# Performance work log

Measured on AMD Instinct MI355X. Metric: run time of the kernel, lower is better.

Reference implementation:

```python
import jax, jax.numpy as jnp
import numpy as np

D_MODEL = 256
EXPERT_DIM = 512
NUM_EXPERTS = 8
TOP_K = 2
SEQ_LEN = 2048
BATCH = 2


def setup_inputs() -> dict:
    key = jax.random.key(0)
    ks = jax.random.split(key, 8)
    s = 0.02
    x = jax.random.normal(ks[0], (SEQ_LEN, BATCH, D_MODEL), dtype=jnp.float32)
    # gate: torch Linear(d_model, num_experts); store as [d, E] so logits = x @ Wg + bg
    Wg = jax.random.normal(ks[1], (D_MODEL, NUM_EXPERTS), dtype=jnp.float32) * s
    bg = jax.random.normal(ks[2], (NUM_EXPERTS,), dtype=jnp.float32) * s
    bias = jnp.zeros((NUM_EXPERTS,), dtype=jnp.float32)  # dynamic routing bias
    # experts: Linear(d, h) -> ReLU -> Linear(h, d), stacked over E
    W1 = jax.random.normal(ks[3], (NUM_EXPERTS, D_MODEL, EXPERT_DIM), dtype=jnp.float32) * s
    b1 = jax.random.normal(ks[4], (NUM_EXPERTS, EXPERT_DIM), dtype=jnp.float32) * s
    W2 = jax.random.normal(ks[5], (NUM_EXPERTS, EXPERT_DIM, D_MODEL), dtype=jnp.float32) * s
    b2 = jax.random.normal(ks[6], (NUM_EXPERTS, D_MODEL), dtype=jnp.float32) * s
    return {"x": x, "Wg": Wg, "bg": bg, "bias": bias, "W1": W1, "b1": b1, "W2": W2, "b2": b2}


def reference(x, Wg, bg, bias, W1, b1, W2, b2):
    # x: [seq, batch, d] -> flatten tokens
    x_flat = x.reshape(-1, D_MODEL)                      # [T, d]
    gate_logits = x_flat @ Wg + bg + bias                # [T, E]
    topk_vals, topk_idx = jax.lax.top_k(gate_logits, TOP_K)   # [T, K]
    # torch code subtracts the row max (topk_vals[:, :1], sorted desc) then softmaxes;
    # jax.nn.softmax is the same stable computation.
    topk_w = jax.nn.softmax(topk_vals, axis=-1)          # [T, K]
    # combine weights over experts: zero for unchosen experts -> exact same math
    # as the masked gather + scatter-add in the original loop.
    combine = (jax.nn.one_hot(topk_idx, NUM_EXPERTS, dtype=x.dtype)
               * topk_w[..., None]).sum(axis=1)          # [T, E]
    h = jax.nn.relu(jnp.einsum('td,edh->teh', x_flat, W1) + b1)   # [T, E, H]
    y = jnp.einsum('teh,ehd->ted', h, W2) + b2                     # [T, E, d]
    out = jnp.einsum('ted,te->td', y, combine)                     # [T, d]
    # dropout is identity in eval mode (p applied only in training)
    return out.reshape(x.shape)
```

## Files before the change

kernel.cpp:

```cpp
#include <hip/hip_runtime.h>
#include <hip/hip_bf16.h>
#include <math.h>

#define D_MODEL 256
#define EXPERT_DIM 512
#define NUM_EXPERTS 8
#define T_TOKENS 4096
#define TM 64
#define NGB 32
#define XS_LD 264

typedef unsigned short ushort_t;
typedef short short8_t __attribute__((ext_vector_type(8)));
typedef float f32x4 __attribute__((ext_vector_type(4)));

__device__ __forceinline__ ushort_t f2bf(float f) {
    unsigned int u = __float_as_uint(f);
    u += 0x7FFFu + ((u >> 16) & 1u);
    return (ushort_t)(u >> 16);
}

__global__ __launch_bounds__(256) void prep_kernel(
    const float* __restrict__ x, const float* __restrict__ Wg,
    const float* __restrict__ bg, const float* __restrict__ bias,
    const float* __restrict__ W1, const float* __restrict__ W2,
    ushort_t* __restrict__ W1f, ushort_t* __restrict__ W2f,
    ushort_t* __restrict__ xb,
    int* __restrict__ gcounts, int* __restrict__ lists,
    float* __restrict__ wts, int* __restrict__ slots)
{
    __shared__ float xs[128][33];
    __shared__ float accbuf[128][9];
    __shared__ int lcount[NUM_EXPERTS];

    const int tid = threadIdx.x;
    if (blockIdx.x < NGB) {
        const int gb = blockIdx.x;
        const int tbase = gb * 128;
        const int tl = tid & 127;
        const int kh = tid >> 7;
        if (tid < NUM_EXPERTS) lcount[tid] = 0;
        float acc[NUM_EXPERTS];
#pragma unroll
        for (int e = 0; e < NUM_EXPERTS; ++e) acc[e] = 0.f;

        for (int kc = 0; kc < 8; ++kc) {
            __syncthreads();
#pragma unroll
            for (int it = 0; it < 4; ++it) {
                int pos = it * 256 + tid;
                int r = pos >> 3, c4 = pos & 7;
                const float* src = x + (size_t)(tbase + r) * D_MODEL + kc * 32 + c4 * 4;
                float4 v = *(const float4*)src;
                xs[r][c4 * 4 + 0] = v.x; xs[r][c4 * 4 + 1] = v.y;
                xs[r][c4 * 4 + 2] = v.z; xs[r][c4 * 4 + 3] = v.w;
                ushort4 o;
                o.x = f2bf(v.x); o.y = f2bf(v.y); o.z = f2bf(v.z); o.w = f2bf(v.w);
                *(ushort4*)&xb[(size_t)(tbase + r) * D_MODEL + kc * 32 + c4 * 4] = o;
            }
            __syncthreads();
            for (int k = kh * 16; k < kh * 16 + 16; ++k) {
                float xv = xs[tl][k];
                const float* wr = Wg + (kc * 32 + k) * NUM_EXPERTS;
#pragma unroll
                for (int e = 0; e < NUM_EXPERTS; ++e) acc[e] += xv * wr[e];
            }
        }
        __syncthreads();
        if (kh == 1) {
#pragma unroll
            for (int e = 0; e < NUM_EXPERTS; ++e) accbuf[tl][e] = acc[e];
        }
        __syncthreads();
        if (kh == 0) {
            float v0 = -3.0e38f, v1 = -3.0e38f; int i0 = 0, i1 = 0;
#pragma unroll
            for (int e = 0; e < NUM_EXPERTS; ++e) {
                float v = acc[e] + accbuf[tl][e] + bg[e] + bias[e];
                if (v > v0) { v1 = v0; i1 = i0; v0 = v; i0 = e; }
                else if (v > v1) { v1 = v; i1 = e; }
            }
            float e1 = __expf(v1 - v0);
            float inv = 1.f / (1.f + e1);
            float w0 = inv, w1 = e1 * inv;

            int p0 = atomicAdd(&lcount[i0], 1);
            int p1 = atomicAdd(&lcount[i1], 1);
            int t = tbase + tl;
            lists[i0 * T_TOKENS + gb * 128 + p0] = t;
            wts  [i0 * T_TOKENS + gb * 128 + p0] = w0;
            lists[i1 * T_TOKENS + gb * 128 + p1] = t;
            wts  [i1 * T_TOKENS + gb * 128 + p1] = w1;
            slots[t] = (i0 << 12 | gb << 7 | p0) | ((i1 << 12 | gb << 7 | p1) << 16);
        }
        __syncthreads();
        if (tid < NUM_EXPERTS) gcounts[gb * NUM_EXPERTS + tid] = lcount[tid];
    } else {
        int gid = (blockIdx.x - NGB) * 256 + tid;
        bool isW2 = gid >= 131072;
        int idx = isW2 ? gid - 131072 : gid;
        int lane = idx & 63;
        int l15 = lane & 15, quad = lane >> 4;
        int ks = (idx >> 6) & 7;
        ushort_t o[8];
        if (!isW2) {
            int ntile = (idx >> 9) & 31, e = idx >> 14;
            int nn = ntile * 16 + l15;
            int k0 = ks * 32 + quad * 8;
            const float* s = W1 + ((size_t)e * D_MODEL + k0) * EXPERT_DIM + nn;
#pragma unroll
            for (int j = 0; j < 8; ++j) o[j] = f2bf(s[j * EXPERT_DIM]);
            *(int4*)(W1f + (size_t)idx * 8) = *(int4*)o;
        } else {
            int ntile = (idx >> 9) & 15, half = (idx >> 13) & 1, e = idx >> 14;
            int nn = ntile * 16 + l15;
            int k0 = half * 256 + ks * 32 + quad * 8;
            const float* s = W2 + ((size_t)e * EXPERT_DIM + k0) * D_MODEL + nn;
#pragma unroll
            for (int j = 0; j < 8; ++j) o[j] = f2bf(s[j * D_MODEL]);
            *(int4*)(W2f + (size_t)idx * 8) = *(int4*)o;
        }
    }
}

__global__ __launch_bounds__(256, 3) void moe_expert_mfma(
    const ushort_t* __restrict__ xb,
    const ushort_t* __restrict__ W1f, const float* __restrict__ b1,
    const ushort_t* __restrict__ W2f, const float* __restrict__ b2,
    const int* __restrict__ gcounts, const int* __restrict__ lists,
    const float* __restrict__ wts, float* __restrict__ ybuf)
{
    const int e = blockIdx.x;
    const int half = blockIdx.y;

    __shared__ ushort_t XH[TM * XS_LD];
    __shared__ int cum[33];
    __shared__ int   toks[TM];
    __shared__ float wt_s[TM];

    const int tid = threadIdx.x;
    if (tid < 32) {
        int v = gcounts[tid * NUM_EXPERTS + e];
#pragma unroll
        for (int s = 1; s < 32; s <<= 1) {
            int u = __shfl_up(v, s, 32);
            if (tid >= s) v += u;
        }
        cum[tid + 1] = v;
        if (tid == 0) cum[0] = 0;
    }
    __syncthreads();
    const int n = cum[32];
    const int base = blockIdx.z * TM;
    if (base >= n) return;
    const int m = min(TM, n - base);

    const int lane = tid & 63;
    const int w = tid >> 6;
    const int l15 = lane & 15;
    const int quad = lane >> 4;

    if (tid < TM) {
        int p = base + tid;
        int tk = -1; float wv = 0.f;
        if (p < n) {
            int lo = 0;
#pragma unroll
            for (int s = 16; s >= 1; s >>= 1) if (cum[lo + s] <= p) lo += s;
            int idx = e * T_TOKENS + lo * 128 + (p - cum[lo]);
            tk = lists[idx]; wv = wts[idx];
        }
        toks[tid] = tk; wt_s[tid] = wv;
    }
    __syncthreads();

    for (int c = tid; c < TM * 32; c += 256) {
        int r = c >> 5, c8 = c & 31;
        int tk = toks[r];
        int4 v = make_int4(0, 0, 0, 0);
        if (tk >= 0) v = *(const int4*)(xb + (size_t)tk * D_MODEL + c8 * 8);
        *(int4*)(XH + r * XS_LD + c8 * 8) = v;
    }
    __syncthreads();

    const ushort_t* W1p = W1f + (size_t)(e * 32 + half * 16 + w * 4) * 4096 + lane * 8;
    float b1v[4];
#pragma unroll
    for (int nt = 0; nt < 4; ++nt)
        b1v[nt] = b1[e * EXPERT_DIM + half * 256 + w * 64 + nt * 16 + l15];

    f32x4 acc1[4][4] = {};
    short8_t bc[4];
#pragma unroll
    for (int nt = 0; nt < 4; ++nt) bc[nt] = *(const short8_t*)(W1p + nt * 4096);

    for (int ks = 0; ks < 8; ++ks) {
        short8_t bn[4];
        if (ks < 7) {
#pragma unroll
            for (int nt = 0; nt < 4; ++nt)
                bn[nt] = *(const short8_t*)(W1p + nt * 4096 + (ks + 1) * 512);
        }
        short8_t a[4];
#pragma unroll
        for (int mt = 0; mt < 4; ++mt)
            a[mt] = *(const short8_t*)(XH + (mt * 16 + l15) * XS_LD + ks * 32 + quad * 8);
#pragma unroll
        for (int mt = 0; mt < 4; ++mt)
#pragma unroll
            for (int nt = 0; nt < 4; ++nt)
                acc1[mt][nt] = __builtin_amdgcn_mfma_f32_16x16x32_bf16(
                    a[mt], bc[nt], acc1[mt][nt], 0, 0, 0);
        if (ks < 7) {
#pragma unroll
            for (int nt = 0; nt < 4; ++nt) bc[nt] = bn[nt];
        }
    }

    const ushort_t* W2p = W2f + (size_t)((e * 2 + half) * 16 + w * 4) * 4096 + lane * 8;
    short8_t bc2[4];
#pragma unroll
    for (int nt = 0; nt < 4; ++nt) bc2[nt] = *(const short8_t*)(W2p + nt * 4096);
    float b2v[4];
#pragma unroll
    for (int nt = 0; nt < 4; ++nt)
        b2v[nt] = half ? b2[e * D_MODEL + w * 64 + nt * 16 + l15] : 0.f;

    __syncthreads();
#pragma unroll
    for (int mt = 0; mt < 4; ++mt)
#pragma unroll
        for (int nt = 0; nt < 4; ++nt)
#pragma unroll
            for (int r = 0; r < 4; ++r) {
                int row = mt * 16 + quad * 4 + r;
                int col = w * 64 + nt * 16 + l15;
                float h = fmaxf(acc1[mt][nt][r] + b1v[nt], 0.f);
                XH[row * XS_LD + col] = f2bf(h);
            }
    __syncthreads();

    f32x4 acc2[4][4] = {};
    for (int ks = 0; ks < 8; ++ks) {
        short8_t bn2[4];
        if (ks < 7) {
#pragma unroll
            for (int nt = 0; nt < 4; ++nt)
                bn2[nt] = *(const short8_t*)(W2p + nt * 4096 + (ks + 1) * 512);
        }
        short8_t a[4];
#pragma unroll
        for (int mt = 0; mt < 4; ++mt)
            a[mt] = *(const short8_t*)(XH + (mt * 16 + l15) * XS_LD + ks * 32 + quad * 8);
#pragma unroll
        for (int mt = 0; mt < 4; ++mt)
#pragma unroll
            for (int nt = 0; nt < 4; ++nt)
                acc2[mt][nt] = __builtin_amdgcn_mfma_f32_16x16x32_bf16(
                    a[mt], bc2[nt], acc2[mt][nt], 0, 0, 0);
        if (ks < 7) {
#pragma unroll
            for (int nt = 0; nt < 4; ++nt) bc2[nt] = bn2[nt];
        }
    }

    float* yrow = ybuf + ((size_t)(half * NUM_EXPERTS + e) * T_TOKENS + base) * D_MODEL;
#pragma unroll
    for (int mt = 0; mt < 4; ++mt)
#pragma unroll
        for (int nt = 0; nt < 4; ++nt)
#pragma unroll
            for (int r = 0; r < 4; ++r) {
                int row = mt * 16 + quad * 4 + r;
                if (row < m) {
                    int col = w * 64 + nt * 16 + l15;
                    yrow[(size_t)row * D_MODEL + col] =
                        wt_s[row] * (acc2[mt][nt][r] + b2v[nt]);
                }
            }
}

__global__ __launch_bounds__(256) void combine_kernel(
    const int* __restrict__ slots, const int* __restrict__ gcounts,
    const float* __restrict__ ybuf, float* __restrict__ out)
{
    __shared__ int cum8[NUM_EXPERTS][33];
    const int tid = threadIdx.x;
    const int lane = tid & 63;
    const int wv = tid >> 6;
    if (lane < 32) {
#pragma unroll
        for (int rpt = 0; rpt < 2; ++rpt) {
            int e = wv + rpt * 4;
            int v = gcounts[lane * NUM_EXPERTS + e];
#pragma unroll
            for (int s = 1; s < 32; s <<= 1) {
                int u = __shfl_up(v, s, 32);
                if (lane >= s) v += u;
            }
            cum8[e][lane + 1] = v;
            if (lane == 0) cum8[e][0] = 0;
        }
    }
    __syncthreads();

    int gid = blockIdx.x * 256 + tid;
    int t = gid >> 6;
    int sl = slots[t];
    int s0 = sl & 0xFFFF, s1 = (sl >> 16) & 0xFFFF;
    int e0 = s0 >> 12, gb0 = (s0 >> 7) & 31, lp0 = s0 & 127;
    int e1 = s1 >> 12, gb1 = (s1 >> 7) & 31, lp1 = s1 & 127;
    int p0 = cum8[e0][gb0] + lp0;
    int p1 = cum8[e1][gb1] + lp1;
    const size_t H = (size_t)NUM_EXPERTS * T_TOKENS * D_MODEL;
    const float4* r0 = (const float4*)(ybuf + ((size_t)e0 * T_TOKENS + p0) * D_MODEL);
    const float4* r1 = (const float4*)(ybuf + ((size_t)e1 * T_TOKENS + p1) * D_MODEL);
    float4 a = r0[lane];
    float4 b = *(const float4*)((const float*)(r0) + H + lane * 4);
    float4 c = r1[lane];
    float4 d = *(const float4*)((const float*)(r1) + H + lane * 4);
    float4 r;
    r.x = a.x + b.x + c.x + d.x;
    r.y = a.y + b.y + c.y + d.y;
    r.z = a.z + b.z + c.z + d.z;
    r.w = a.w + b.w + c.w + d.w;
    ((float4*)(out + (size_t)t * D_MODEL))[lane] = r;
}

extern "C" void kernel_launch(void* const* d_in, const int* in_sizes, int n_in,
                              void* d_out, int out_size, void* d_ws, size_t ws_size,
                              hipStream_t stream)
{
    const float* x    = (const float*)d_in[0];
    const float* Wg   = (const float*)d_in[1];
    const float* bg   = (const float*)d_in[2];
    const float* bias = (const float*)d_in[3];
    const float* W1   = (const float*)d_in[4];
    const float* b1   = (const float*)d_in[5];
    const float* W2   = (const float*)d_in[6];
    const float* b2   = (const float*)d_in[7];
    float* out = (float*)d_out;

    char* ws = (char*)d_ws;
    int*      gcounts = (int*)ws;
    int*      lists   = (int*)(ws + 1024);
    float*    wts     = (float*)(ws + 132096);
    int*      slots   = (int*)(ws + 263168);
    ushort_t* xb      = (ushort_t*)(ws + 524288);
    ushort_t* W1f     = (ushort_t*)(ws + 2621440);
    ushort_t* W2f     = (ushort_t*)(ws + 4718592);
    float*    ybuf    = (float*)(ws + 6815744);

    prep_kernel<<<1056, 256, 0, stream>>>(
        x, Wg, bg, bias, W1, W2, W1f, W2f, xb, gcounts, lists, wts, slots);

    moe_expert_mfma<<<dim3(NUM_EXPERTS, 2, T_TOKENS / TM), 256, 0, stream>>>(
        xb, W1f, b1, W2f, b2, gcounts, lists, wts, ybuf);

    combine_kernel<<<T_TOKENS * 64 / 256, 256, 0, stream>>>(slots, gcounts, ybuf, out);
}
```

Before: 115.4 us.

## Spread gating over 256 small blocks and store expert outputs in bf16

Measured after the change: 104.6 us. 9.4% less time.

```diff
diff --git a/kernel.cpp b/kernel.cpp
--- a/kernel.cpp
+++ b/kernel.cpp
@@ -7,7 +7,7 @@
 #define NUM_EXPERTS 8
 #define T_TOKENS 4096
 #define TM 64
-#define NGB 32
+#define NGB 256
 #define XS_LD 264
 
 typedef unsigned short ushort_t;
@@ -18,6 +18,9 @@
     unsigned int u = __float_as_uint(f);
     u += 0x7FFFu + ((u >> 16) & 1u);
     return (ushort_t)(u >> 16);
+}
+__device__ __forceinline__ float bf2f(ushort_t u) {
+    return __uint_as_float((unsigned int)u << 16);
 }
 
 __global__ __launch_bounds__(256) void prep_kernel(
@@ -29,54 +32,55 @@
     int* __restrict__ gcounts, int* __restrict__ lists,
     float* __restrict__ wts, int* __restrict__ slots)
 {
-    __shared__ float xs[128][33];
-    __shared__ float accbuf[128][9];
     __shared__ int lcount[NUM_EXPERTS];
-
     const int tid = threadIdx.x;
+
     if (blockIdx.x < NGB) {
         const int gb = blockIdx.x;
-        const int tbase = gb * 128;
-        const int tl = tid & 127;
-        const int kh = tid >> 7;
+        const int r = tid >> 4;
+        const int c = tid & 15;
+        const int t = gb * 16 + r;
         if (tid < NUM_EXPERTS) lcount[tid] = 0;
+
+        float xr[16];
+        const float4* xp = (const float4*)(x + (size_t)t * D_MODEL + c * 16);
+#pragma unroll
+        for (int q = 0; q < 4; ++q) {
+            float4 v = xp[q];
+            xr[q * 4 + 0] = v.x; xr[q * 4 + 1] = v.y;
+            xr[q * 4 + 2] = v.z; xr[q * 4 + 3] = v.w;
+        }
+        ushort_t o16[16];
+#pragma unroll
+        for (int j = 0; j < 16; ++j) o16[j] = f2bf(xr[j]);
+        ushort_t* xbp = xb + (size_t)t * D_MODEL + c * 16;
+        *(int4*)(xbp)     = *(int4*)(o16);
+        *(int4*)(xbp + 8) = *(int4*)(o16 + 8);
+
         float acc[NUM_EXPERTS];
 #pragma unroll
         for (int e = 0; e < NUM_EXPERTS; ++e) acc[e] = 0.f;
-
-        for (int kc = 0; kc < 8; ++kc) {
-            __syncthreads();
-#pragma unroll
-            for (int it = 0; it < 4; ++it) {
-                int pos = it * 256 + tid;
-                int r = pos >> 3, c4 = pos & 7;
-                const float* src = x + (size_t)(tbase + r) * D_MODEL + kc * 32 + c4 * 4;
-                float4 v = *(const float4*)src;
-                xs[r][c4 * 4 + 0] = v.x; xs[r][c4 * 4 + 1] = v.y;
-                xs[r][c4 * 4 + 2] = v.z; xs[r][c4 * 4 + 3] = v.w;
-                ushort4 o;
-                o.x = f2bf(v.x); o.y = f2bf(v.y); o.z = f2bf(v.z); o.w = f2bf(v.w);
-                *(ushort4*)&xb[(size_t)(tbase + r) * D_MODEL + kc * 32 + c4 * 4] = o;
-            }
-            __syncthreads();
-            for (int k = kh * 16; k < kh * 16 + 16; ++k) {
-                float xv = xs[tl][k];
-                const float* wr = Wg + (kc * 32 + k) * NUM_EXPERTS;
-#pragma unroll
-                for (int e = 0; e < NUM_EXPERTS; ++e) acc[e] += xv * wr[e];
-            }
+#pragma unroll
+        for (int j = 0; j < 16; ++j) {
+            const float4* wg = (const float4*)(Wg + (c * 16 + j) * NUM_EXPERTS);
+            float4 w0 = wg[0], w1 = wg[1];
+            float xv = xr[j];
+            acc[0] += xv * w0.x; acc[1] += xv * w0.y;
+            acc[2] += xv * w0.z; acc[3] += xv * w0.w;
+            acc[4] += xv * w1.x; acc[5] += xv * w1.y;
+            acc[6] += xv * w1.z; acc[7] += xv * w1.w;
+        }
+#pragma unroll
+        for (int e = 0; e < NUM_EXPERTS; ++e) {
+#pragma unroll
+            for (int s = 1; s < 16; s <<= 1) acc[e] += __shfl_xor(acc[e], s);
         }
         __syncthreads();
-        if (kh == 1) {
-#pragma unroll
-            for (int e = 0; e < NUM_EXPERTS; ++e) accbuf[tl][e] = acc[e];
-        }
-        __syncthreads();
-        if (kh == 0) {
+        if (c == 0) {
             float v0 = -3.0e38f, v1 = -3.0e38f; int i0 = 0, i1 = 0;
 #pragma unroll
             for (int e = 0; e < NUM_EXPERTS; ++e) {
-                float v = acc[e] + accbuf[tl][e] + bg[e] + bias[e];
+                float v = acc[e] + bg[e] + bias[e];
                 if (v > v0) { v1 = v0; i1 = i0; v0 = v; i0 = e; }
                 else if (v > v1) { v1 = v; i1 = e; }
             }
@@ -86,12 +90,11 @@
 
             int p0 = atomicAdd(&lcount[i0], 1);
             int p1 = atomicAdd(&lcount[i1], 1);
-            int t = tbase + tl;
-            lists[i0 * T_TOKENS + gb * 128 + p0] = t;
-            wts  [i0 * T_TOKENS + gb * 128 + p0] = w0;
-            lists[i1 * T_TOKENS + gb * 128 + p1] = t;
-            wts  [i1 * T_TOKENS + gb * 128 + p1] = w1;
-            slots[t] = (i0 << 12 | gb << 7 | p0) | ((i1 << 12 | gb << 7 | p1) << 16);
+            lists[i0 * T_TOKENS + gb * 16 + p0] = t;
+            wts  [i0 * T_TOKENS + gb * 16 + p0] = w0;
+            lists[i1 * T_TOKENS + gb * 16 + p1] = t;
+            wts  [i1 * T_TOKENS + gb * 16 + p1] = w1;
+            slots[t] = (i0 << 12 | gb << 4 | p0) | ((i1 << 12 | gb << 4 | p1) << 16);
         }
         __syncthreads();
         if (tid < NUM_EXPERTS) gcounts[gb * NUM_EXPERTS + tid] = lcount[tid];
@@ -128,37 +131,42 @@
     const ushort_t* __restrict__ W1f, const float* __restrict__ b1,
     const ushort_t* __restrict__ W2f, const float* __restrict__ b2,
     const int* __restrict__ gcounts, const int* __restrict__ lists,
-    const float* __restrict__ wts, float* __restrict__ ybuf)
+    const float* __restrict__ wts, ushort_t* __restrict__ ybuf)
 {
     const int e = blockIdx.x;
     const int half = blockIdx.y;
 
     __shared__ ushort_t XH[TM * XS_LD];
-    __shared__ int cum[33];
+    __shared__ int cum[257];
+    __shared__ int wsums[4];
     __shared__ int   toks[TM];
     __shared__ float wt_s[TM];
 
     const int tid = threadIdx.x;
-    if (tid < 32) {
-        int v = gcounts[tid * NUM_EXPERTS + e];
-#pragma unroll
-        for (int s = 1; s < 32; s <<= 1) {
-            int u = __shfl_up(v, s, 32);
-            if (tid >= s) v += u;
-        }
-        cum[tid + 1] = v;
-        if (tid == 0) cum[0] = 0;
-    }
-    __syncthreads();
-    const int n = cum[32];
-    const int base = blockIdx.z * TM;
-    if (base >= n) return;
-    const int m = min(TM, n - base);
-
     const int lane = tid & 63;
     const int w = tid >> 6;
     const int l15 = lane & 15;
     const int quad = lane >> 4;
+
+    {
+        int v = gcounts[tid * NUM_EXPERTS + e];
+#pragma unroll
+        for (int s = 1; s < 64; s <<= 1) {
+            int u = __shfl_up(v, s);
+            if (lane >= s) v += u;
+        }
+        if (lane == 63) wsums[w] = v;
+        __syncthreads();
+        int off = 0;
+        for (int i = 0; i < w; ++i) off += wsums[i];
+        cum[tid + 1] = v + off;
+        if (tid == 0) cum[0] = 0;
+        __syncthreads();
+    }
+    const int n = cum[256];
+    const int base = blockIdx.z * TM;
+    if (base >= n) return;
+    const int m = min(TM, n - base);
 
     if (tid < TM) {
         int p = base + tid;
@@ -166,8 +174,9 @@
         if (p < n) {
             int lo = 0;
 #pragma unroll
-            for (int s = 16; s >= 1; s >>= 1) if (cum[lo + s] <= p) lo += s;
-            int idx = e * T_TOKENS + lo * 128 + (p - cum[lo]);
+            for (int s = 128; s >= 1; s >>= 1)
+                if (cum[lo + s] <= p) lo += s;
+            int idx = e * T_TOKENS + lo * 16 + (p - cum[lo]);
             tk = lists[idx]; wv = wts[idx];
         }
         toks[tid] = tk; wt_s[tid] = wv;
@@ -264,7 +273,7 @@
         }
     }
 
-    float* yrow = ybuf + ((size_t)(half * NUM_EXPERTS + e) * T_TOKENS + base) * D_MODEL;
+    ushort_t* yrow = ybuf + ((size_t)(half * NUM_EXPERTS + e) * T_TOKENS + base) * D_MODEL;
 #pragma unroll
     for (int mt = 0; mt < 4; ++mt)
 #pragma unroll
@@ -275,32 +284,35 @@
                 if (row < m) {
                     int col = w * 64 + nt * 16 + l15;
                     yrow[(size_t)row * D_MODEL + col] =
-                        wt_s[row] * (acc2[mt][nt][r] + b2v[nt]);
+                        f2bf(wt_s[row] * (acc2[mt][nt][r] + b2v[nt]));
                 }
             }
 }
 
 __global__ __launch_bounds__(256) void combine_kernel(
     const int* __restrict__ slots, const int* __restrict__ gcounts,
-    const float* __restrict__ ybuf, float* __restrict__ out)
+    const ushort_t* __restrict__ ybuf, float* __restrict__ out)
 {
-    __shared__ int cum8[NUM_EXPERTS][33];
+    __shared__ int cum8[NUM_EXPERTS][257];
     const int tid = threadIdx.x;
     const int lane = tid & 63;
     const int wv = tid >> 6;
-    if (lane < 32) {
-#pragma unroll
-        for (int rpt = 0; rpt < 2; ++rpt) {
-            int e = wv + rpt * 4;
-            int v = gcounts[lane * NUM_EXPERTS + e];
-#pragma unroll
-            for (int s = 1; s < 32; s <<= 1) {
-                int u = __shfl_up(v, s, 32);
+#pragma unroll
+    for (int rpt = 0; rpt < 2; ++rpt) {
+        int e = wv + rpt * 4;
+        int carry = 0;
+        for (int ch = 0; ch < 4; ++ch) {
+            int v = gcounts[(ch * 64 + lane) * NUM_EXPERTS + e];
+#pragma unroll
+            for (int s = 1; s < 64; s <<= 1) {
+                int u = __shfl_up(v, s);
                 if (lane >= s) v += u;
             }
-            cum8[e][lane + 1] = v;
-            if (lane == 0) cum8[e][0] = 0;
-        }
+            v += carry;
+            cum8[e][ch * 64 + lane + 1] = v;
+            carry = __shfl(v, 63);
+        }
+        if (lane == 0) cum8[e][0] = 0;
     }
     __syncthreads();
 
@@ -308,23 +320,23 @@
     int t = gid >> 6;
     int sl = slots[t];
     int s0 = sl & 0xFFFF, s1 = (sl >> 16) & 0xFFFF;
-    int e0 = s0 >> 12, gb0 = (s0 >> 7) & 31, lp0 = s0 & 127;
-    int e1 = s1 >> 12, gb1 = (s1 >> 7) & 31, lp1 = s1 & 127;
-    int p0 = cum8[e0][gb0] + lp0;
-    int p1 = cum8[e1][gb1] + lp1;
+    int e0 = (s0 >> 12) & 7, g0 = (s0 >> 4) & 255, lp0 = s0 & 15;
+    int e1 = (s1 >> 12) & 7, g1 = (s1 >> 4) & 255, lp1 = s1 & 15;
+    int p0 = cum8[e0][g0] + lp0;
+    int p1 = cum8[e1][g1] + lp1;
     const size_t H = (size_t)NUM_EXPERTS * T_TOKENS * D_MODEL;
-    const float4* r0 = (const float4*)(ybuf + ((size_t)e0 * T_TOKENS + p0) * D_MODEL);
-    const float4* r1 = (const float4*)(ybuf + ((size_t)e1 * T_TOKENS + p1) * D_MODEL);
-    float4 a = r0[lane];
-    float4 b = *(const float4*)((const float*)(r0) + H + lane * 4);
-    float4 c = r1[lane];
-    float4 d = *(const float4*)((const float*)(r1) + H + lane * 4);
+    size_t o0 = ((size_t)e0 * T_TOKENS + p0) * D_MODEL + lane * 4;
+    size_t o1 = ((size_t)e1 * T_TOKENS + p1) * D_MODEL + lane * 4;
+    ushort4 a = *(const ushort4*)(ybuf + o0);
+    ushort4 b = *(const ushort4*)(ybuf + o0 + H);
+    ushort4 c = *(const ushort4*)(ybuf + o1);
+    ushort4 d = *(const ushort4*)(ybuf + o1 + H);
     float4 r;
-    r.x = a.x + b.x + c.x + d.x;
-    r.y = a.y + b.y + c.y + d.y;
-    r.z = a.z + b.z + c.z + d.z;
-    r.w = a.w + b.w + c.w + d.w;
-    ((float4*)(out + (size_t)t * D_MODEL))[lane] = r;
+    r.x = bf2f(a.x) + bf2f(b.x) + bf2f(c.x) + bf2f(d.x);
+    r.y = bf2f(a.y) + bf2f(b.y) + bf2f(c.y) + bf2f(d.y);
+    r.z = bf2f(a.z) + bf2f(b.z) + bf2f(c.z) + bf2f(d.z);
+    r.w = bf2f(a.w) + bf2f(b.w) + bf2f(c.w) + bf2f(d.w);
+    *(float4*)(out + (size_t)t * D_MODEL + lane * 4) = r;
 }
 
 extern "C" void kernel_launch(void* const* d_in, const int* in_sizes, int n_in,
@@ -343,15 +355,15 @@
 
     char* ws = (char*)d_ws;
     int*      gcounts = (int*)ws;
-    int*      lists   = (int*)(ws + 1024);
-    float*    wts     = (float*)(ws + 132096);
-    int*      slots   = (int*)(ws + 263168);
+    int*      lists   = (int*)(ws + 8192);
+    float*    wts     = (float*)(ws + 139264);
+    int*      slots   = (int*)(ws + 270336);
     ushort_t* xb      = (ushort_t*)(ws + 524288);
     ushort_t* W1f     = (ushort_t*)(ws + 2621440);
     ushort_t* W2f     = (ushort_t*)(ws + 4718592);
-    float*    ybuf    = (float*)(ws + 6815744);
-
-    prep_kernel<<<1056, 256, 0, stream>>>(
+    ushort_t* ybuf    = (ushort_t*)(ws + 6815744);
+
+    prep_kernel<<<NGB + 1024, 256, 0, stream>>>(
         x, Wg, bg, bias, W1, W2, W1f, W2f, xb, gcounts, lists, wts, slots);
 
     moe_expert_mfma<<<dim3(NUM_EXPERTS, 2, T_TOKENS / TM), 256, 0, stream>>>(
```
